# Kernel tuning notes

Hardware: AMD Instinct MI355X
Metric: run time of the kernel (lower is better)

The kernel has to match this reference:

```python
import jax, jax.numpy as jnp
import numpy as np

DIM = 1024
NUM_HEADS = 16
HEAD_DIM = DIM // NUM_HEADS
GATE_HID = DIM // 4


def setup_inputs() -> dict:
    key = jax.random.key(0)
    ks = jax.random.split(key, 16)
    B, S, D = 2, 2048, DIM
    sc = 1.0 / np.sqrt(D)
    inp = {
        "h": jax.random.normal(ks[0], (B, S, D), jnp.float32),
        "x": jax.random.normal(ks[1], (B, S, D), jnp.float32),
        # attention projections, stored (in, out) so y = x @ W + b
        "Wq": jax.random.normal(ks[2], (D, D), jnp.float32) * sc,
        "bq": jnp.zeros((D,), jnp.float32),
        "Wk": jax.random.normal(ks[3], (D, D), jnp.float32) * sc,
        "bk": jnp.zeros((D,), jnp.float32),
        "Wv": jax.random.normal(ks[4], (D, D), jnp.float32) * sc,
        "bv": jnp.zeros((D,), jnp.float32),
        "Wo": jax.random.normal(ks[5], (D, D), jnp.float32) * sc,
        "bo": jnp.zeros((D,), jnp.float32),
        # gating MLP: Linear(2D -> D//4) -> GELU -> Linear(D//4 -> D) -> sigmoid
        "Wg1": jax.random.normal(ks[6], (2 * D, GATE_HID), jnp.float32) * (1.0 / np.sqrt(2 * D)),
        "bg1": jnp.zeros((GATE_HID,), jnp.float32),
        "Wg2": jax.random.normal(ks[7], (GATE_HID, D), jnp.float32) * (1.0 / np.sqrt(GATE_HID)),
        "bg2": jnp.zeros((D,), jnp.float32),
    }
    return inp


def reference(h, x, Wq, bq, Wk, bk, Wv, bv, Wo, bo, Wg1, bg1, Wg2, bg2):
    B, S, D = h.shape
    # gated blend of latent h and input x
    gate_in = jnp.concatenate([h, x], axis=-1)                      # (B,S,2D)
    gate = jax.nn.sigmoid((jax.nn.gelu(gate_in @ Wg1 + bg1, approximate=False)) @ Wg2 + bg2)
    blended = gate * h + (1.0 - gate) * x                           # (B,S,D)
    # multi-head self-attention
    q = (blended @ Wq + bq).reshape(B, S, NUM_HEADS, HEAD_DIM)
    k = (blended @ Wk + bk).reshape(B, S, NUM_HEADS, HEAD_DIM)
    v = (blended @ Wv + bv).reshape(B, S, NUM_HEADS, HEAD_DIM)
    scale = 1.0 / np.sqrt(HEAD_DIM).astype(np.float32)
    scores = jnp.einsum('bqhd,bkhd->bhqk', q, k) * scale            # (B,H,S,S)
    attn = jax.nn.softmax(scores, axis=-1)
    out = jnp.einsum('bhqk,bkhd->bqhd', attn, v).reshape(B, S, D)
    return out @ Wo + bo
```

## Files before the change

### kernel.cpp

```cpp
#include <hip/hip_runtime.h>
#include <hip/hip_bf16.h>


typedef __attribute__((ext_vector_type(4))) unsigned int u32x4;
typedef __attribute__((ext_vector_type(2))) unsigned int u32x2;
typedef __attribute__((ext_vector_type(8))) short s16x8;
typedef __attribute__((ext_vector_type(8))) unsigned short u16x8;
typedef __attribute__((ext_vector_type(4))) float f32x4;

#define QSCALE 0.18033688011112043f
#define FIXED_M 24.0f

__device__ __forceinline__ unsigned short f2bf(float f) {
    unsigned int i = __builtin_bit_cast(unsigned int, f) + 0x8000u;
    return (unsigned short)(i >> 16);
}
__device__ __forceinline__ unsigned int pack2bf(float a, float b) {
    unsigned int ia = __builtin_bit_cast(unsigned int, a) + 0x8000u;
    unsigned int ib = __builtin_bit_cast(unsigned int, b) + 0x8000u;
    return __builtin_amdgcn_perm(ib, ia, 0x07060302u);
}

__device__ __forceinline__ void gload16(const void* g, void* l) {
    __builtin_amdgcn_global_load_lds(
        (const __attribute__((address_space(1))) void*)g,
        (__attribute__((address_space(3))) void*)l, 16, 0, 0);
}

struct TEntry { const float* src; unsigned short* dst; int K; int N; };
struct TTable { TEntry e[6]; };

__global__ __launch_bounds__(256) void prep_all(
    TTable tt,
    const float* __restrict__ h, const float* __restrict__ x,
    unsigned short* __restrict__ hx,
    const float* __restrict__ bq, const float* __restrict__ bk,
    const float* __restrict__ bv, float* __restrict__ bqkv)
{
    const int bid = (int)blockIdx.x;
    if (bid < 6144) {
        const TEntry E = tt.e[bid >> 10];
        const int bx = bid & 1023;
        const int ntn = E.N >> 5;
        if (bx >= (E.K >> 5) * ntn) return;
        const int n0 = (bx % ntn) * 32, k0 = (bx / ntn) * 32;
        __shared__ float tile[32][33];
        const int tx = threadIdx.x & 31, ty = threadIdx.x >> 5;
#pragma unroll
        for (int i = 0; i < 4; ++i)
            tile[ty + i * 8][tx] = E.src[(size_t)(k0 + ty + i * 8) * E.N + n0 + tx];
        __syncthreads();
#pragma unroll
        for (int i = 0; i < 4; ++i)
            E.dst[(size_t)(n0 + ty + i * 8) * E.K + k0 + tx] = f2bf(tile[tx][ty + i * 8]);
        return;
    }
    if (bid < 6144 + 4096) {
        const int idx = (bid - 6144) * 256 + threadIdx.x;
        const size_t e = (size_t)idx * 8;
        const int r = (int)(e >> 11), c = (int)(e & 2047);
        const float* src = (c < 1024) ? (h + (size_t)r * 1024 + c)
                                      : (x + (size_t)r * 1024 + (c - 1024));
        u16x8 o;
#pragma unroll
        for (int j = 0; j < 8; ++j) o[j] = f2bf(src[j]);
        *reinterpret_cast<u16x8*>(hx + e) = o;
        return;
    }
    const int i = (bid - 6144 - 4096) * 256 + threadIdx.x;
    if (i < 1024) bqkv[i] = bq[i];
    else if (i < 2048) bqkv[i] = bk[i - 1024];
    else if (i < 3072) bqkv[i] = bv[i - 2048];
}

__global__ __launch_bounds__(256) void transpose_v(
    const unsigned short* __restrict__ qkv, unsigned short* __restrict__ vt)
{
    __shared__ unsigned short t[64][65];
    const int st = blockIdx.x;
    const int bh = blockIdx.y;
    const int b = bh >> 4, h = bh & 15;
    const int tx = threadIdx.x & 63, ty = threadIdx.x >> 6;
    const int s0 = st * 64;
    const size_t base = (size_t)(b * 2048 + s0) * 3072 + 2048 + h * 64;
#pragma unroll
    for (int i = 0; i < 16; ++i)
        t[ty + i * 4][tx] = qkv[base + (size_t)(ty + i * 4) * 3072 + tx];
    __syncthreads();
    const size_t obase = (size_t)(bh * 64) * 2048 + s0;
#pragma unroll
    for (int i = 0; i < 16; ++i)
        vt[obase + (size_t)(ty + i * 4) * 2048 + tx] = t[tx][ty + i * 4];
}

enum { EPI_GELU = 1, EPI_BLEND = 2, EPI_F32 = 3, EPI_QKV = 4 };

template <int EPI>
__global__ __launch_bounds__(256, 2) void gemm_kernel(
    const unsigned short* __restrict__ A, int lda,
    const unsigned short* __restrict__ Bt, int ldb,
    const float* __restrict__ bias,
    void* __restrict__ Cv, int ldc, int K,
    const float* __restrict__ hb, const float* __restrict__ xb,
    int swzn, int ntn)
{
    __shared__ unsigned short Alds[2][128 * 32];
    __shared__ unsigned short Blds[2][128 * 32];

    const int tid = threadIdx.x;
    const int lane = tid & 63;
    const int w = tid >> 6;
    const int wr = w >> 1, wc = w & 1;
    int mt, nt;
    if (swzn > 0) {
        const int xcd = (int)blockIdx.x & 7, seq = (int)blockIdx.x >> 3;
        nt = xcd * swzn + seq % swzn;
        mt = seq / swzn;
    } else {
        nt = (int)blockIdx.x % ntn;
        mt = (int)blockIdx.x / ntn;
    }
    const int m0 = mt * 128, n0 = nt * 128;
    const int lrow = lane & 15, lko = (lane >> 4) * 8;

    const int grow = w * 32 + (lane >> 2);
    const int gk8 = (lane & 3) * 8;
    const unsigned short* ga0 = A + (size_t)(m0 + grow) * lda + gk8;
    const unsigned short* ga1 = ga0 + (size_t)16 * lda;
    const unsigned short* gb0 = Bt + (size_t)(n0 + grow) * ldb + gk8;
    const unsigned short* gb1 = gb0 + (size_t)16 * ldb;

    auto stage = [&](int buf, int k0) {
        unsigned short* la = &Alds[buf][w * 1024];
        unsigned short* lb = &Blds[buf][w * 1024];
        gload16(ga0 + k0, la);
        gload16(ga1 + k0, la + 512);
        gload16(gb0 + k0, lb);
        gload16(gb1 + k0, lb + 512);
    };

    f32x4 acc[4][4];
#pragma unroll
    for (int i = 0; i < 4; ++i)
#pragma unroll
        for (int j = 0; j < 4; ++j) acc[i][j] = (f32x4){0.f, 0.f, 0.f, 0.f};

    const int kks = K >> 5;
    stage(0, 0);
    __syncthreads();

    for (int t = 0; t < kks; ++t) {
        const int cur = t & 1;
        if (t + 1 < kks) stage(cur ^ 1, (t + 1) << 5);

        s16x8 af[4], bfr[4];
#pragma unroll
        for (int mi = 0; mi < 4; ++mi)
            af[mi] = *reinterpret_cast<const s16x8*>(&Alds[cur][(wr * 64 + mi * 16 + lrow) * 32 + lko]);
#pragma unroll
        for (int ni = 0; ni < 4; ++ni)
            bfr[ni] = *reinterpret_cast<const s16x8*>(&Blds[cur][(wc * 64 + ni * 16 + lrow) * 32 + lko]);
#pragma unroll
        for (int mi = 0; mi < 4; ++mi)
#pragma unroll
            for (int ni = 0; ni < 4; ++ni)
                acc[mi][ni] = __builtin_amdgcn_mfma_f32_16x16x32_bf16(af[mi], bfr[ni], acc[mi][ni], 0, 0, 0);

        __syncthreads();
    }

    const int rbase = m0 + wr * 64;
    const int cbase = n0 + wc * 64;
#pragma unroll
    for (int mi = 0; mi < 4; ++mi) {
#pragma unroll
        for (int j = 0; j < 4; ++j) {
            const int r = rbase + mi * 16 + (lane >> 4) * 4 + j;
#pragma unroll
            for (int ni = 0; ni < 4; ++ni) {
                const int c = cbase + ni * 16 + (lane & 15);
                float v = acc[mi][ni][j] + bias[c];
                if constexpr (EPI == EPI_GELU) {
                    float g = 0.5f * v * (1.f + erff(v * 0.70710678118654752f));
                    ((unsigned short*)Cv)[(size_t)r * ldc + c] = f2bf(g);
                } else if constexpr (EPI == EPI_BLEND) {
                    float gate = 1.f / (1.f + __expf(-v));
                    const size_t o = (size_t)r * ldc + c;
                    float bl = gate * hb[o] + (1.f - gate) * xb[o];
                    ((unsigned short*)Cv)[o] = f2bf(bl);
                } else if constexpr (EPI == EPI_QKV) {
                    const float scl = (c < 1024) ? QSCALE : 1.f;
                    ((unsigned short*)Cv)[(size_t)r * ldc + c] = f2bf(v * scl);
                } else {
                    ((float*)Cv)[(size_t)r * ldc + c] = v;
                }
            }
        }
    }
}

__global__ __launch_bounds__(256, 2) void gemm_gelu64(
    const unsigned short* __restrict__ A, int lda,
    const unsigned short* __restrict__ Bt, int ldb,
    const float* __restrict__ bias,
    unsigned short* __restrict__ C, int ldc, int K)
{
    __shared__ unsigned short Alds[2][64 * 32];
    __shared__ unsigned short Blds[2][64 * 32];

    const int tid = threadIdx.x;
    const int lane = tid & 63;
    const int w = tid >> 6;
    const int wr = w >> 1, wc = w & 1;
    const int nt = (int)blockIdx.x & 3, mt = (int)blockIdx.x >> 2;
    const int m0 = mt * 64, n0 = nt * 64;
    const int lrow = lane & 15, lko = (lane >> 4) * 8;

    const int grow = w * 16 + (lane >> 2);
    const int gk8 = (lane & 3) * 8;
    const unsigned short* ga = A + (size_t)(m0 + grow) * lda + gk8;
    const unsigned short* gb = Bt + (size_t)(n0 + grow) * ldb + gk8;

    auto stage = [&](int buf, int k0) {
        gload16(ga + k0, &Alds[buf][w * 512]);
        gload16(gb + k0, &Blds[buf][w * 512]);
    };

    f32x4 acc[2][2];
#pragma unroll
    for (int i = 0; i < 2; ++i)
#pragma unroll
        for (int j = 0; j < 2; ++j) acc[i][j] = (f32x4){0.f, 0.f, 0.f, 0.f};

    const int kks = K >> 5;
    stage(0, 0);
    __syncthreads();

    for (int t = 0; t < kks; ++t) {
        const int cur = t & 1;
        if (t + 1 < kks) stage(cur ^ 1, (t + 1) << 5);

        s16x8 af[2], bfr[2];
#pragma unroll
        for (int mi = 0; mi < 2; ++mi)
            af[mi] = *reinterpret_cast<const s16x8*>(&Alds[cur][(wr * 32 + mi * 16 + lrow) * 32 + lko]);
#pragma unroll
        for (int ni = 0; ni < 2; ++ni)
            bfr[ni] = *reinterpret_cast<const s16x8*>(&Blds[cur][(wc * 32 + ni * 16 + lrow) * 32 + lko]);
#pragma unroll
        for (int mi = 0; mi < 2; ++mi)
#pragma unroll
            for (int ni = 0; ni < 2; ++ni)
                acc[mi][ni] = __builtin_amdgcn_mfma_f32_16x16x32_bf16(af[mi], bfr[ni], acc[mi][ni], 0, 0, 0);

        __syncthreads();
    }

    const int rbase = m0 + wr * 32;
    const int cbase = n0 + wc * 32;
#pragma unroll
    for (int mi = 0; mi < 2; ++mi) {
#pragma unroll
        for (int j = 0; j < 4; ++j) {
            const int r = rbase + mi * 16 + (lane >> 4) * 4 + j;
#pragma unroll
            for (int ni = 0; ni < 2; ++ni) {
                const int c = cbase + ni * 16 + (lane & 15);
                float v = acc[mi][ni][j] + bias[c];
                float g = 0.5f * v * (1.f + erff(v * 0.70710678118654752f));
                C[(size_t)r * ldc + c] = f2bf(g);
            }
        }
    }
}

#define ALD 72

__global__ __launch_bounds__(512, 4) void attn_kernel(
    const unsigned short* __restrict__ qkv,
    const unsigned short* __restrict__ vt,
    unsigned short* __restrict__ out)
{
    __shared__ unsigned short Klds[2][64 * ALD];
    __shared__ unsigned short Vlds[2][64 * ALD];
    __shared__ unsigned short Plds[8][16 * ALD];

    const int tid = threadIdx.x, lane = tid & 63, w = tid >> 6;
    const int xcd = (int)blockIdx.x & 7, seq = (int)blockIdx.x >> 3;
    const int bh = xcd * 4 + (seq & 3);
    const int qt = seq >> 2;
    const int b = bh >> 4, h = bh & 15;
    const int rb = b * 2048;
    const int lrow = lane & 15, g = lane >> 4, lko = g * 8;

    s16x8 qf[2];
    {
        const size_t qrow = (size_t)(rb + qt * 128 + w * 16 + lrow) * 3072 + h * 64;
        qf[0] = *reinterpret_cast<const s16x8*>(qkv + qrow + lko);
        qf[1] = *reinterpret_cast<const s16x8*>(qkv + qrow + 32 + lko);
    }

    const int srow = tid >> 3, sc8 = (tid & 7) * 8;
    const unsigned short* kp = qkv + (size_t)(rb + srow) * 3072 + 1024 + h * 64 + sc8;
    const unsigned short* vp = vt + (size_t)(bh * 64 + srow) * 2048 + sc8;

    u32x4 kreg, vreg;
    auto stage_load = [&](int t0) {
        kreg = *reinterpret_cast<const u32x4*>(kp + (size_t)t0 * 3072);
        vreg = *reinterpret_cast<const u32x4*>(vp + t0);
    };
    auto stage_write = [&](int buf) {
        *reinterpret_cast<u32x4*>(&Klds[buf][srow * ALD + sc8]) = kreg;
        *reinterpret_cast<u32x4*>(&Vlds[buf][srow * ALD + sc8]) = vreg;
    };

    f32x4 acc[4];
#pragma unroll
    for (int di = 0; di < 4; ++di) acc[di] = (f32x4){0.f, 0.f, 0.f, 0.f};
    float lsum = 0.f;

    unsigned short* pw = &Plds[w][0];

    stage_load(0);
    stage_write(0);
    stage_load(64);
    __syncthreads();

    for (int t0 = 0; t0 < 2048; t0 += 64) {
        const int cur = (t0 >> 6) & 1;

        f32x4 s[4];
#pragma unroll
        for (int ni = 0; ni < 4; ++ni) s[ni] = (f32x4){0.f, 0.f, 0.f, 0.f};
#pragma unroll
        for (int ni = 0; ni < 4; ++ni)
#pragma unroll
            for (int fi = 0; fi < 2; ++fi) {
                s16x8 kf = *reinterpret_cast<const s16x8*>(&Klds[cur][(ni * 16 + lrow) * ALD + fi * 32 + lko]);
                s[ni] = __builtin_amdgcn_mfma_f32_16x16x32_bf16(kf, qf[fi], s[ni], 0, 0, 0);
            }

        if (t0 + 64 < 2048) stage_write(cur ^ 1);
        if (t0 + 128 < 2048) stage_load(t0 + 128);

#pragma unroll
        for (int ni = 0; ni < 4; ++ni) {
            float p0 = __builtin_amdgcn_exp2f(s[ni][0] - FIXED_M);
            float p1 = __builtin_amdgcn_exp2f(s[ni][1] - FIXED_M);
            float p2 = __builtin_amdgcn_exp2f(s[ni][2] - FIXED_M);
            float p3 = __builtin_amdgcn_exp2f(s[ni][3] - FIXED_M);
            lsum += (p0 + p1) + (p2 + p3);
            u32x2 pk = {pack2bf(p0, p1), pack2bf(p2, p3)};
            *reinterpret_cast<u32x2*>(&pw[lrow * ALD + ni * 16 + g * 4]) = pk;
        }

#pragma unroll
        for (int st = 0; st < 2; ++st) {
            s16x8 pf = *reinterpret_cast<const s16x8*>(&pw[lrow * ALD + st * 32 + lko]);
#pragma unroll
            for (int di = 0; di < 4; ++di) {
                s16x8 vf = *reinterpret_cast<const s16x8*>(&Vlds[cur][(di * 16 + lrow) * ALD + st * 32 + lko]);
                acc[di] = __builtin_amdgcn_mfma_f32_16x16x32_bf16(vf, pf, acc[di], 0, 0, 0);
            }
        }

        __syncthreads();
    }

    lsum += __shfl_xor(lsum, 16);
    lsum += __shfl_xor(lsum, 32);
    const float inv = 1.f / lsum;
    const size_t orow = (size_t)(rb + qt * 128 + w * 16 + lrow) * 1024 + h * 64;
#pragma unroll
    for (int di = 0; di < 4; ++di) {
        u32x2 ov = {pack2bf(acc[di][0] * inv, acc[di][1] * inv),
                    pack2bf(acc[di][2] * inv, acc[di][3] * inv)};
        *reinterpret_cast<u32x2*>(&out[orow + di * 16 + g * 4]) = ov;
    }
}

extern "C" void kernel_launch(void* const* d_in, const int* in_sizes, int n_in,
                              void* d_out, int out_size, void* d_ws, size_t ws_size,
                              hipStream_t stream)
{
    const float* h   = (const float*)d_in[0];
    const float* x   = (const float*)d_in[1];
    const float* Wq  = (const float*)d_in[2];
    const float* bq  = (const float*)d_in[3];
    const float* Wk  = (const float*)d_in[4];
    const float* bk  = (const float*)d_in[5];
    const float* Wv  = (const float*)d_in[6];
    const float* bv  = (const float*)d_in[7];
    const float* Wo  = (const float*)d_in[8];
    const float* bo  = (const float*)d_in[9];
    const float* Wg1 = (const float*)d_in[10];
    const float* bg1 = (const float*)d_in[11];
    const float* Wg2 = (const float*)d_in[12];
    const float* bg2 = (const float*)d_in[13];

    char* ws = (char*)d_ws;
    size_t off = 0;
    auto alloc = [&](size_t bytes) {
        void* p = ws + off;
        off += (bytes + 255) & ~(size_t)255;
        return p;
    };
    unsigned short* wg1T  = (unsigned short*)alloc((size_t)256 * 2048 * 2);
    unsigned short* wg2T  = (unsigned short*)alloc((size_t)1024 * 256 * 2);
    unsigned short* wqkvT = (unsigned short*)alloc((size_t)3072 * 1024 * 2);
    unsigned short* woT   = (unsigned short*)alloc((size_t)1024 * 1024 * 2);
    float*          bqkv  = (float*)alloc((size_t)3072 * 4);
    unsigned short* blend = (unsigned short*)alloc((size_t)4096 * 1024 * 2);
    unsigned short* attno = (unsigned short*)alloc((size_t)4096 * 1024 * 2);
    unsigned short* vtb   = (unsigned short*)alloc((size_t)32 * 64 * 2048 * 2);
    char* uni = (char*)alloc((size_t)4096 * 3072 * 2);
    unsigned short* hx  = (unsigned short*)uni;
    unsigned short* g1  = (unsigned short*)(uni + (size_t)4096 * 2048 * 2);
    unsigned short* qkv = (unsigned short*)uni;
    (void)ws_size; (void)in_sizes; (void)n_in; (void)out_size;

    TTable tt;
    tt.e[0] = {Wg1, wg1T, 2048, 256};
    tt.e[1] = {Wg2, wg2T, 256, 1024};
    tt.e[2] = {Wq, wqkvT, 1024, 1024};
    tt.e[3] = {Wk, wqkvT + (size_t)1024 * 1024, 1024, 1024};
    tt.e[4] = {Wv, wqkvT + (size_t)2048 * 1024, 1024, 1024};
    tt.e[5] = {Wo, woT, 1024, 1024};
    prep_all<<<6144 + 4096 + 12, 256, 0, stream>>>(tt, h, x, hx, bq, bk, bv, bqkv);

    gemm_gelu64<<<256, 256, 0, stream>>>(hx, 2048, wg1T, 2048, bg1, g1, 256, 2048);
    gemm_kernel<EPI_BLEND><<<256, 256, 0, stream>>>(
        g1, 256, wg2T, 256, bg2, blend, 1024, 256, h, x, 1, 8);

    gemm_kernel<EPI_QKV><<<768, 256, 0, stream>>>(
        blend, 1024, wqkvT, 1024, bqkv, qkv, 3072, 1024, nullptr, nullptr, 3, 24);

    transpose_v<<<dim3(32, 32), 256, 0, stream>>>(qkv, vtb);

    attn_kernel<<<512, 512, 0, stream>>>(qkv, vtb, attno);

    gemm_kernel<EPI_F32><<<256, 256, 0, stream>>>(
        attno, 1024, woT, 1024, bo, (float*)d_out, 1024, 1024, nullptr, nullptr, 1, 8);
}
```

Baseline: 175.9 us.

## Process two query tiles per warp in attention to reuse K/V fragments

Each warp in the attention kernel now handles 32 query rows as two 16-row groups instead of 16 rows. The K and V fragments loaded from LDS are shared by both groups, and the grid is halved to 256 blocks. This cuts LDS reads and global K/V staging per query row, and gives more independent MFMA work between the exp and P write/read steps. In exchange it raises register pressure (launch bounds relaxed to 2) and leaves only one block per CU, which lowers occupancy and latency hiding.

```diff
diff --git a/kernel.cpp b/kernel.cpp
--- a/kernel.cpp
+++ b/kernel.cpp
@@ -276,7 +276,7 @@
 
 #define ALD 72
 
-__global__ __launch_bounds__(512, 4) void attn_kernel(
+__global__ __launch_bounds__(512, 2) void attn_kernel(
     const unsigned short* __restrict__ qkv,
     const unsigned short* __restrict__ vt,
     unsigned short* __restrict__ out)
@@ -293,11 +293,12 @@
     const int rb = b * 2048;
     const int lrow = lane & 15, g = lane >> 4, lko = g * 8;
 
-    s16x8 qf[2];
-    {
-        const size_t qrow = (size_t)(rb + qt * 128 + w * 16 + lrow) * 3072 + h * 64;
-        qf[0] = *reinterpret_cast<const s16x8*>(qkv + qrow + lko);
-        qf[1] = *reinterpret_cast<const s16x8*>(qkv + qrow + 32 + lko);
+    s16x8 qf[2][2];
+#pragma unroll
+    for (int qg = 0; qg < 2; ++qg) {
+        const size_t qrow = (size_t)(rb + qt * 256 + w * 32 + qg * 16 + lrow) * 3072 + h * 64;
+        qf[qg][0] = *reinterpret_cast<const s16x8*>(qkv + qrow + lko);
+        qf[qg][1] = *reinterpret_cast<const s16x8*>(qkv + qrow + 32 + lko);
     }
 
     const int srow = tid >> 3, sc8 = (tid & 7) * 8;
@@ -314,10 +315,13 @@
         *reinterpret_cast<u32x4*>(&Vlds[buf][srow * ALD + sc8]) = vreg;
     };
 
-    f32x4 acc[4];
-#pragma unroll
-    for (int di = 0; di < 4; ++di) acc[di] = (f32x4){0.f, 0.f, 0.f, 0.f};
-    float lsum = 0.f;
+    f32x4 acc0[4], acc1[4];
+#pragma unroll
+    for (int di = 0; di < 4; ++di) {
+        acc0[di] = (f32x4){0.f, 0.f, 0.f, 0.f};
+        acc1[di] = (f32x4){0.f, 0.f, 0.f, 0.f};
+    }
+    float lsum0 = 0.f, lsum1 = 0.f;
 
     unsigned short* pw = &Plds[w][0];
 
@@ -329,53 +333,100 @@
     for (int t0 = 0; t0 < 2048; t0 += 64) {
         const int cur = (t0 >> 6) & 1;
 
-        f32x4 s[4];
-#pragma unroll
-        for (int ni = 0; ni < 4; ++ni) s[ni] = (f32x4){0.f, 0.f, 0.f, 0.f};
+        s16x8 kf[4][2];
 #pragma unroll
         for (int ni = 0; ni < 4; ++ni)
 #pragma unroll
-            for (int fi = 0; fi < 2; ++fi) {
-                s16x8 kf = *reinterpret_cast<const s16x8*>(&Klds[cur][(ni * 16 + lrow) * ALD + fi * 32 + lko]);
-                s[ni] = __builtin_amdgcn_mfma_f32_16x16x32_bf16(kf, qf[fi], s[ni], 0, 0, 0);
-            }
+            for (int fi = 0; fi < 2; ++fi)
+                kf[ni][fi] = *reinterpret_cast<const s16x8*>(
+                    &Klds[cur][(ni * 16 + lrow) * ALD + fi * 32 + lko]);
+
+        f32x4 s0[4];
+#pragma unroll
+        for (int ni = 0; ni < 4; ++ni) s0[ni] = (f32x4){0.f, 0.f, 0.f, 0.f};
+#pragma unroll
+        for (int ni = 0; ni < 4; ++ni)
+#pragma unroll
+            for (int fi = 0; fi < 2; ++fi)
+                s0[ni] = __builtin_amdgcn_mfma_f32_16x16x32_bf16(kf[ni][fi], qf[0][fi], s0[ni], 0, 0, 0);
 
         if (t0 + 64 < 2048) stage_write(cur ^ 1);
         if (t0 + 128 < 2048) stage_load(t0 + 128);
 
 #pragma unroll
         for (int ni = 0; ni < 4; ++ni) {
-            float p0 = __builtin_amdgcn_exp2f(s[ni][0] - FIXED_M);
-            float p1 = __builtin_amdgcn_exp2f(s[ni][1] - FIXED_M);
-            float p2 = __builtin_amdgcn_exp2f(s[ni][2] - FIXED_M);
-            float p3 = __builtin_amdgcn_exp2f(s[ni][3] - FIXED_M);
-            lsum += (p0 + p1) + (p2 + p3);
+            float p0 = __builtin_amdgcn_exp2f(s0[ni][0] - FIXED_M);
+            float p1 = __builtin_amdgcn_exp2f(s0[ni][1] - FIXED_M);
+            float p2 = __builtin_amdgcn_exp2f(s0[ni][2] - FIXED_M);
+            float p3 = __builtin_amdgcn_exp2f(s0[ni][3] - FIXED_M);
+            lsum0 += (p0 + p1) + (p2 + p3);
             u32x2 pk = {pack2bf(p0, p1), pack2bf(p2, p3)};
             *reinterpret_cast<u32x2*>(&pw[lrow * ALD + ni * 16 + g * 4]) = pk;
         }
 
+        f32x4 s1[4];
+#pragma unroll
+        for (int ni = 0; ni < 4; ++ni) s1[ni] = (f32x4){0.f, 0.f, 0.f, 0.f};
+#pragma unroll
+        for (int ni = 0; ni < 4; ++ni)
+#pragma unroll
+            for (int fi = 0; fi < 2; ++fi)
+                s1[ni] = __builtin_amdgcn_mfma_f32_16x16x32_bf16(kf[ni][fi], qf[1][fi], s1[ni], 0, 0, 0);
+
+        s16x8 vf[2][4];
+#pragma unroll
+        for (int st = 0; st < 2; ++st)
+#pragma unroll
+            for (int di = 0; di < 4; ++di)
+                vf[st][di] = *reinterpret_cast<const s16x8*>(
+                    &Vlds[cur][(di * 16 + lrow) * ALD + st * 32 + lko]);
+
 #pragma unroll
         for (int st = 0; st < 2; ++st) {
             s16x8 pf = *reinterpret_cast<const s16x8*>(&pw[lrow * ALD + st * 32 + lko]);
 #pragma unroll
-            for (int di = 0; di < 4; ++di) {
-                s16x8 vf = *reinterpret_cast<const s16x8*>(&Vlds[cur][(di * 16 + lrow) * ALD + st * 32 + lko]);
-                acc[di] = __builtin_amdgcn_mfma_f32_16x16x32_bf16(vf, pf, acc[di], 0, 0, 0);
-            }
+            for (int di = 0; di < 4; ++di)
+                acc0[di] = __builtin_amdgcn_mfma_f32_16x16x32_bf16(vf[st][di], pf, acc0[di], 0, 0, 0);
+        }
+
+#pragma unroll
+        for (int ni = 0; ni < 4; ++ni) {
+            float p0 = __builtin_amdgcn_exp2f(s1[ni][0] - FIXED_M);
+            float p1 = __builtin_amdgcn_exp2f(s1[ni][1] - FIXED_M);
+            float p2 = __builtin_amdgcn_exp2f(s1[ni][2] - FIXED_M);
+            float p3 = __builtin_amdgcn_exp2f(s1[ni][3] - FIXED_M);
+            lsum1 += (p0 + p1) + (p2 + p3);
+            u32x2 pk = {pack2bf(p0, p1), pack2bf(p2, p3)};
+            *reinterpret_cast<u32x2*>(&pw[lrow * ALD + ni * 16 + g * 4]) = pk;
+        }
+
+#pragma unroll
+        for (int st = 0; st < 2; ++st) {
+            s16x8 pf = *reinterpret_cast<const s16x8*>(&pw[lrow * ALD + st * 32 + lko]);
+#pragma unroll
+            for (int di = 0; di < 4; ++di)
+                acc1[di] = __builtin_amdgcn_mfma_f32_16x16x32_bf16(vf[st][di], pf, acc1[di], 0, 0, 0);
         }
 
         __syncthreads();
     }
 
-    lsum += __shfl_xor(lsum, 16);
-    lsum += __shfl_xor(lsum, 32);
-    const float inv = 1.f / lsum;
-    const size_t orow = (size_t)(rb + qt * 128 + w * 16 + lrow) * 1024 + h * 64;
+    lsum0 += __shfl_xor(lsum0, 16);
+    lsum0 += __shfl_xor(lsum0, 32);
+    lsum1 += __shfl_xor(lsum1, 16);
+    lsum1 += __shfl_xor(lsum1, 32);
+    const float inv0 = 1.f / lsum0;
+    const float inv1 = 1.f / lsum1;
+    const size_t orow0 = (size_t)(rb + qt * 256 + w * 32 + lrow) * 1024 + h * 64;
+    const size_t orow1 = orow0 + (size_t)16 * 1024;
 #pragma unroll
     for (int di = 0; di < 4; ++di) {
-        u32x2 ov = {pack2bf(acc[di][0] * inv, acc[di][1] * inv),
-                    pack2bf(acc[di][2] * inv, acc[di][3] * inv)};
-        *reinterpret_cast<u32x2*>(&out[orow + di * 16 + g * 4]) = ov;
+        u32x2 ov0 = {pack2bf(acc0[di][0] * inv0, acc0[di][1] * inv0),
+                     pack2bf(acc0[di][2] * inv0, acc0[di][3] * inv0)};
+        *reinterpret_cast<u32x2*>(&out[orow0 + di * 16 + g * 4]) = ov0;
+        u32x2 ov1 = {pack2bf(acc1[di][0] * inv1, acc1[di][1] * inv1),
+                     pack2bf(acc1[di][2] * inv1, acc1[di][3] * inv1)};
+        *reinterpret_cast<u32x2*>(&out[orow1 + di * 16 + g * 4]) = ov1;
     }
 }
 
@@ -437,7 +488,7 @@
 
     transpose_v<<<dim3(32, 32), 256, 0, stream>>>(qkv, vtb);
 
-    attn_kernel<<<512, 512, 0, stream>>>(qkv, vtb, attno);
+    attn_kernel<<<256, 512, 0, stream>>>(qkv, vtb, attno);
 
     gemm_kernel<EPI_F32><<<256, 256, 0, stream>>>(
         attno, 1024, woT, 1024, bo, (float*)d_out, 1024, 1024, nullptr, nullptr, 1, 8);
```

After: 173.0 us. No clear change (-1.7%).
